# Optimization experiments

Measured on AMD Instinct MI355X. Metric: run time of the kernel, lower is better.

## Reference

```python
import jax, jax.numpy as jnp
import numpy as np

EPS = 0.01  # the module uses 1/sqrt(||x||^2 + 0.01) for cosine normalization


def setup_inputs() -> dict:
    key = jax.random.key(0)
    k1, k2, k3, k4, k5, k6 = jax.random.split(key, 6)
    B, L, L1, D = 512, 256, 256, 128
    sequence = jax.random.randint(k1, (B, L), 0, 10000, dtype=jnp.int32)
    last_sequence = jax.random.randint(k2, (B, L), 0, 2, dtype=jnp.int32)
    sequence_1 = jax.random.randint(k3, (B, L1), 0, 10000, dtype=jnp.int32)
    hist_1 = jax.random.normal(k4, (B, L, D), dtype=jnp.float32)
    hist_2 = jax.random.normal(k5, (B, L1, D), dtype=jnp.float32)
    W = jax.random.normal(k6, (D, D), dtype=jnp.float32) * (1.0 / np.sqrt(D))
    return {"sequence": sequence, "last_sequence": last_sequence,
            "sequence_1": sequence_1, "hist_1": hist_1, "hist_2": hist_2, "W": W}


def reference(sequence, last_sequence, sequence_1, hist_1, hist_2, W):
    # Masks: nonzero ids -> 1.0 (cast to bool then float in the original)
    m = (sequence != 0).astype(jnp.float32)        # [B, L]   key mask for self-attn
    m1 = (sequence_1 != 0).astype(jnp.float32)     # [B, L1]  key mask for cross-attn
    last = last_sequence.astype(jnp.float32)       # [B, L]   last-position indicator

    # --- self cosine-similarity attention over hist_1 ---
    # cos[b,i,j] = <hist_1[b,i], hist_1[b,j]> / (sqrt(||h_i||^2+eps) * sqrt(||h_j||^2+eps))
    dots = jnp.einsum('bid,bjd->bij', hist_1, hist_1)            # [B, L, L]
    inv = jax.lax.rsqrt(jnp.sum(hist_1 * hist_1, axis=-1) + EPS)  # [B, L]
    cos = dots * inv[:, :, None] * inv[:, None, :]
    # softmax-style weighting: exp(cos) masked over keys j (unnormalized exp, per original)
    w = jnp.exp(cos) * m[:, None, :]                             # [B, L, L]
    wsum = jnp.sum(w, axis=-1)                                   # [B, L]
    h_self = jnp.einsum('bij,bjd->bid', w, hist_1) / wsum[..., None]  # [B, L, D]

    # residual add, mask by query validity, then pool at the 'last' position
    h_all_add = (h_self + hist_1) * m[..., None]                 # [B, L, D]
    h_last = jnp.sum(h_all_add * last[..., None], axis=1)        # [B, D]

    # --- cross cosine-similarity attention: h_last attends over hist_2 ---
    dots2 = jnp.einsum('bkd,bd->bk', hist_2, h_last)             # [B, L1]
    inv2k = jax.lax.rsqrt(jnp.sum(hist_2 * hist_2, axis=-1) + EPS)  # [B, L1]
    inv2q = jax.lax.rsqrt(jnp.sum(h_last * h_last, axis=-1) + EPS)  # [B]
    cos2 = dots2 * inv2k * inv2q[:, None]
    w2 = jnp.exp(cos2) * m1                                      # [B, L1]
    h = jnp.einsum('bk,bkd->bd', w2, hist_2) / jnp.sum(w2, axis=-1, keepdims=True)

    out = jax.nn.relu(h @ W)                                     # [B, D]
    return out.reshape(-1, 1, W.shape[0])                        # [B, 1, hidden_num]
```

## Files before the change

### kernel.cpp

```cpp
#include <hip/hip_runtime.h>


using u16 = unsigned short;
using u32 = unsigned int;
typedef __attribute__((ext_vector_type(8))) short bf16x8;
typedef __attribute__((ext_vector_type(4))) float f32x4;
typedef __attribute__((ext_vector_type(4))) u32 u32x4;
typedef __attribute__((ext_vector_type(2))) u32 u32x2;

#define KST 136
#define TST 40
#define WSTR 40
#define KBSZ 4352
#define TBSZ 5120

__device__ __forceinline__ u16 f2bf(float f) {
  union { float f; u32 i; } v; v.f = f;
  u32 r = v.i + 0x7FFFu + ((v.i >> 16) & 1u);
  return (u16)(r >> 16);
}
__device__ __forceinline__ bf16x8 as_bf(u32x4 x) {
  union { u32x4 u; bf16x8 b; } c; c.u = x; return c.b;
}
__device__ __forceinline__ u32x4 pack_bf8(const float* p, float& ss) {
  const float4 a = *(const float4*)p;
  const float4 c = *(const float4*)(p + 4);
  ss += a.x*a.x + a.y*a.y + a.z*a.z + a.w*a.w
      + c.x*c.x + c.y*c.y + c.z*c.z + c.w*c.w;
  u32x4 v;
  v.x = (u32)f2bf(a.x) | ((u32)f2bf(a.y) << 16);
  v.y = (u32)f2bf(a.z) | ((u32)f2bf(a.w) << 16);
  v.z = (u32)f2bf(c.x) | ((u32)f2bf(c.y) << 16);
  v.w = (u32)f2bf(c.z) | ((u32)f2bf(c.w) << 16);
  return v;
}
__device__ __forceinline__ u32x4 packpair(float4 a, float4 c) {
  u32x4 v;
  v.x = (u32)f2bf(a.x) | ((u32)f2bf(a.y) << 16);
  v.y = (u32)f2bf(a.z) | ((u32)f2bf(a.w) << 16);
  v.z = (u32)f2bf(c.x) | ((u32)f2bf(c.y) << 16);
  v.w = (u32)f2bf(c.z) | ((u32)f2bf(c.w) << 16);
  return v;
}

__device__ __forceinline__ void stage_tile(u32x4 v, float ss, u16* kb, u16* tb,
                                           float* invt, int wv, int q, int m16) {
  const int row = wv * 4 + q;
  *(u32x4*)&kb[row * KST + m16 * 8] = v;
  ss += __shfl_xor(ss, 1); ss += __shfl_xor(ss, 2);
  ss += __shfl_xor(ss, 4); ss += __shfl_xor(ss, 8);
  if (m16 == 0) invt[row] = rsqrtf(ss + 0.01f);
  u32 w0 = v.x, w1 = v.y, w2 = v.z, w3 = v.w;
  {
    const int s1 = q & 1;
    u32 xa = s1 ? w0 : w1;
    u32 xb = s1 ? w2 : w3;
    xa = __shfl_xor(xa, 16);
    xb = __shfl_xor(xb, 16);
    if (s1) { w0 = xa; w2 = xb; } else { w1 = xa; w3 = xb; }
    const int s2 = q >> 1;
    u32 ya = s2 ? w0 : w2;
    u32 yb = s2 ? w1 : w3;
    ya = __shfl_xor(ya, 32);
    yb = __shfl_xor(yb, 32);
    if (s2) { w0 = ya; w1 = yb; } else { w2 = ya; w3 = yb; }
  }
  const int d0   = m16 * 8 + q * 2;
  const int base = wv * 4;
  u32x2 lo; lo.x = (w0 & 0xffffu) | (w1 << 16); lo.y = (w2 & 0xffffu) | (w3 << 16);
  u32x2 hi; hi.x = (w0 >> 16) | (w1 & 0xffff0000u); hi.y = (w2 >> 16) | (w3 & 0xffff0000u);
  *(u32x2*)&tb[d0 * TST + base]       = lo;
  *(u32x2*)&tb[(d0 + 1) * TST + base] = hi;
}

__launch_bounds__(512)
__global__ void itd_fused(const int* __restrict__ seq,
                          const int* __restrict__ lastseq,
                          const int* __restrict__ seq1,
                          const float* __restrict__ h1g,
                          const float* __restrict__ h2g,
                          const float* __restrict__ wg,
                          float* __restrict__ outg) {
  __shared__ unsigned long long SBIG[4736];
  __shared__ u16 WST[8][2 * 16 * WSTR];
  __shared__ float MK[256], LM[256], HLacc[128], HH[128], INVT[64], SC[2];

  u16* const  Kb  = (u16*)SBIG;
  u16* const  Tb  = (u16*)SBIG + 2 * KBSZ;
  float* const PSC = (float*)SBIG;

  const int b    = blockIdx.x;
  const int t    = threadIdx.x;
  const int lane = t & 63;
  const int wv   = t >> 6;
  const int q    = lane >> 4;
  const int m16  = lane & 15;

  const float* h1b = h1g + (size_t)b * 32768;

  if (t < 128) HLacc[t] = 0.f;
  if (t < 256) {
    float m = (seq[b * 256 + t] != 0) ? 1.f : 0.f;
    MK[t] = m;
    LM[t] = m * (float)lastseq[b * 256 + t];
  }

  u32x4 av[2][4];
  float invi[2][4];
  #pragma unroll
  for (int rt = 0; rt < 2; ++rt) {
    const int i0 = wv * 32 + rt * 16;
    float ss = 0.f;
    #pragma unroll
    for (int s = 0; s < 4; ++s)
      av[rt][s] = pack_bf8(&h1b[(i0 + m16) * 128 + s * 32 + q * 8], ss);
    ss += __shfl_xor(ss, 16);
    ss += __shfl_xor(ss, 32);
    const float invrow = rsqrtf(ss + 0.01f);
    #pragma unroll
    for (int r = 0; r < 4; ++r) invi[rt][r] = __shfl(invrow, q * 4 + r);
  }

  __syncthreads();

  const int srow = t >> 4;
  const int scol = (t & 15) * 8;
  float4 rpA = {0.f, 0.f, 0.f, 0.f};
  float4 rpB = {0.f, 0.f, 0.f, 0.f};
  {
    const float4 a0 = *(const float4*)&h1b[srow * 128 + scol];
    const float4 c0 = *(const float4*)&h1b[srow * 128 + scol + 4];
    const float lm0 = LM[srow];
    rpA.x += lm0 * a0.x; rpA.y += lm0 * a0.y; rpA.z += lm0 * a0.z; rpA.w += lm0 * a0.w;
    rpB.x += lm0 * c0.x; rpB.y += lm0 * c0.y; rpB.z += lm0 * c0.z; rpB.w += lm0 * c0.w;
    float ss = a0.x*a0.x + a0.y*a0.y + a0.z*a0.z + a0.w*a0.w
             + c0.x*c0.x + c0.y*c0.y + c0.z*c0.z + c0.w*c0.w;
    stage_tile(packpair(a0, c0), ss, Kb, Tb, INVT, wv, q, m16);
  }
  __syncthreads();

  const f32x4 fz = {0.f, 0.f, 0.f, 0.f};
  f32x4 acc[2][8];
  #pragma unroll
  for (int rt = 0; rt < 2; ++rt)
    #pragma unroll
    for (int dt = 0; dt < 8; ++dt) acc[rt][dt] = fz;
  float wpart[2][4] = {{0.f,0.f,0.f,0.f},{0.f,0.f,0.f,0.f}};
  u16* wst0 = &WST[wv][0];
  u16* wst1 = &WST[wv][16 * WSTR];

  for (int jt = 0; jt < 8; ++jt) {
    const int cur = jt & 1;
    float4 pfa, pfb;
    if (jt < 7) {
      const float* np = &h1b[(jt + 1) * 4096 + srow * 128 + scol];
      pfa = *(const float4*)np;
      pfb = *(const float4*)(np + 4);
    }

    f32x4 Sa[2] = {fz, fz}, Sb[2] = {fz, fz};
    const u16* kb = Kb + cur * KBSZ;
    #pragma unroll
    for (int s = 0; s < 4; ++s) {
      bf16x8 ba = *(const bf16x8*)&kb[m16 * KST + s * 32 + q * 8];
      bf16x8 bb = *(const bf16x8*)&kb[(16 + m16) * KST + s * 32 + q * 8];
      bf16x8 a0 = as_bf(av[0][s]);
      bf16x8 a1 = as_bf(av[1][s]);
      Sa[0] = __builtin_amdgcn_mfma_f32_16x16x32_bf16(a0, ba, Sa[0], 0, 0, 0);
      Sb[0] = __builtin_amdgcn_mfma_f32_16x16x32_bf16(a0, bb, Sb[0], 0, 0, 0);
      Sa[1] = __builtin_amdgcn_mfma_f32_16x16x32_bf16(a1, ba, Sa[1], 0, 0, 0);
      Sb[1] = __builtin_amdgcn_mfma_f32_16x16x32_bf16(a1, bb, Sb[1], 0, 0, 0);
    }
    const float invja = INVT[cur * 32 + m16];
    const float invjb = INVT[cur * 32 + 16 + m16];
    const float mja = MK[jt * 32 + m16];
    const float mjb = MK[jt * 32 + 16 + m16];
    #pragma unroll
    for (int rt = 0; rt < 2; ++rt) {
      u16* wr = rt ? wst1 : wst0;
      #pragma unroll
      for (int r = 0; r < 4; ++r) {
        const float wa = __expf(Sa[rt][r] * (invi[rt][r] * invja)) * mja;
        const float wb = __expf(Sb[rt][r] * (invi[rt][r] * invjb)) * mjb;
        wpart[rt][r] += wa + wb;
        wr[(q * 4 + r) * WSTR + m16]      = f2bf(wa);
        wr[(q * 4 + r) * WSTR + 16 + m16] = f2bf(wb);
      }
    }
    __threadfence_block();
    const bf16x8 aw0 = *(const bf16x8*)&wst0[m16 * WSTR + q * 8];
    const bf16x8 aw1 = *(const bf16x8*)&wst1[m16 * WSTR + q * 8];
    const u16* tb = Tb + cur * TBSZ;
    #pragma unroll
    for (int dt = 0; dt < 8; ++dt) {
      const bf16x8 bt = *(const bf16x8*)&tb[(dt * 16 + m16) * TST + q * 8];
      acc[0][dt] = __builtin_amdgcn_mfma_f32_16x16x32_bf16(aw0, bt, acc[0][dt], 0, 0, 0);
      acc[1][dt] = __builtin_amdgcn_mfma_f32_16x16x32_bf16(aw1, bt, acc[1][dt], 0, 0, 0);
    }
    if (jt < 7) {
      const float lmrow = LM[(jt + 1) * 32 + srow];
      rpA.x += lmrow * pfa.x; rpA.y += lmrow * pfa.y;
      rpA.z += lmrow * pfa.z; rpA.w += lmrow * pfa.w;
      rpB.x += lmrow * pfb.x; rpB.y += lmrow * pfb.y;
      rpB.z += lmrow * pfb.z; rpB.w += lmrow * pfb.w;
      float ss = pfa.x*pfa.x + pfa.y*pfa.y + pfa.z*pfa.z + pfa.w*pfa.w
               + pfb.x*pfb.x + pfb.y*pfb.y + pfb.z*pfb.z + pfb.w*pfb.w;
      stage_tile(packpair(pfa, pfb), ss,
                 Kb + (cur ^ 1) * KBSZ, Tb + (cur ^ 1) * TBSZ,
                 INVT + (cur ^ 1) * 32, wv, q, m16);
    }
    __syncthreads();
  }

  #pragma unroll
  for (int rt = 0; rt < 2; ++rt) {
    const int i0 = wv * 32 + rt * 16;
    float rws[4];
    #pragma unroll
    for (int r = 0; r < 4; ++r) {
      float s = wpart[rt][r];
      s += __shfl_xor(s, 1); s += __shfl_xor(s, 2);
      s += __shfl_xor(s, 4); s += __shfl_xor(s, 8);
      rws[r] = 1.f / s;
    }
    #pragma unroll
    for (int dt = 0; dt < 8; ++dt) {
      float v = 0.f;
      #pragma unroll
      for (int r = 0; r < 4; ++r)
        v += acc[rt][dt][r] * rws[r] * LM[i0 + q * 4 + r];
      v += __shfl_xor(v, 16);
      v += __shfl_xor(v, 32);
      if (q == 0) atomicAdd(&HLacc[dt * 16 + m16], v);
    }
  }

  *(float4*)&PSC[srow * 132 + scol]     = rpA;
  *(float4*)&PSC[srow * 132 + scol + 4] = rpB;
  __syncthreads();
  if (t < 128) {
    float s = 0.f;
    #pragma unroll 8
    for (int n = 0; n < 32; ++n) s += PSC[n * 132 + t];
    HLacc[t] += s;
  }
  __syncthreads();

  if (t < 64) {
    float s = HLacc[t] * HLacc[t] + HLacc[t + 64] * HLacc[t + 64];
    s += __shfl_xor(s, 1); s += __shfl_xor(s, 2); s += __shfl_xor(s, 4);
    s += __shfl_xor(s, 8); s += __shfl_xor(s, 16); s += __shfl_xor(s, 32);
    if (t == 0) SC[0] = rsqrtf(s + 0.01f);
  }
  if (t < 256) MK[t] = (seq1[b * 256 + t] != 0) ? 1.f : 0.f;
  __syncthreads();

  const float* h2b = h2g + (size_t)b * 32768;
  {
    const int row8 = lane >> 3;
    const int sub  = lane & 7;
    const int slot = wv * 8 + row8;
    const float invq = SC[0];
    float4 acc4[4];
    #pragma unroll
    for (int c = 0; c < 4; ++c) acc4[c] = {0.f, 0.f, 0.f, 0.f};
    float ws2 = 0.f;
    const float* hl = &HLacc[sub * 4];
    #pragma unroll
    for (int kt = 0; kt < 4; ++kt) {
      const int k = kt * 64 + slot;
      const float* rowp = h2b + k * 128 + sub * 4;
      const float4 v0 = *(const float4*)(rowp);
      const float4 v1 = *(const float4*)(rowp + 32);
      const float4 v2 = *(const float4*)(rowp + 64);
      const float4 v3 = *(const float4*)(rowp + 96);
      float dot = v0.x*hl[0]  + v0.y*hl[1]  + v0.z*hl[2]  + v0.w*hl[3]
                + v1.x*hl[32] + v1.y*hl[33] + v1.z*hl[34] + v1.w*hl[35]
                + v2.x*hl[64] + v2.y*hl[65] + v2.z*hl[66] + v2.w*hl[67]
                + v3.x*hl[96] + v3.y*hl[97] + v3.z*hl[98] + v3.w*hl[99];
      float ss  = v0.x*v0.x + v0.y*v0.y + v0.z*v0.z + v0.w*v0.w
                + v1.x*v1.x + v1.y*v1.y + v1.z*v1.z + v1.w*v1.w
                + v2.x*v2.x + v2.y*v2.y + v2.z*v2.z + v2.w*v2.w
                + v3.x*v3.x + v3.y*v3.y + v3.z*v3.z + v3.w*v3.w;
      dot += __shfl_xor(dot, 1); dot += __shfl_xor(dot, 2); dot += __shfl_xor(dot, 4);
      ss  += __shfl_xor(ss, 1);  ss  += __shfl_xor(ss, 2);  ss  += __shfl_xor(ss, 4);
      const float w2 = __expf(dot * rsqrtf(ss + 0.01f) * invq) * MK[k];
      ws2 += w2;
      acc4[0].x += w2*v0.x; acc4[0].y += w2*v0.y; acc4[0].z += w2*v0.z; acc4[0].w += w2*v0.w;
      acc4[1].x += w2*v1.x; acc4[1].y += w2*v1.y; acc4[1].z += w2*v1.z; acc4[1].w += w2*v1.w;
      acc4[2].x += w2*v2.x; acc4[2].y += w2*v2.y; acc4[2].z += w2*v2.z; acc4[2].w += w2*v2.w;
      acc4[3].x += w2*v3.x; acc4[3].y += w2*v3.y; acc4[3].z += w2*v3.z; acc4[3].w += w2*v3.w;
    }
    #pragma unroll
    for (int c = 0; c < 4; ++c)
      *(float4*)&PSC[slot * 132 + c * 32 + sub * 4] = acc4[c];
    if (sub == 0) INVT[slot] = ws2;
  }
  __syncthreads();

  float hsum = 0.f;
  if (t < 128) {
    #pragma unroll 8
    for (int n = 0; n < 64; ++n) hsum += PSC[n * 132 + t];
  }
  if (t < 64) {
    float s = INVT[t];
    s += __shfl_xor(s, 1); s += __shfl_xor(s, 2); s += __shfl_xor(s, 4);
    s += __shfl_xor(s, 8); s += __shfl_xor(s, 16); s += __shfl_xor(s, 32);
    if (t == 0) SC[1] = s;
  }
  __syncthreads();
  if (t < 128) HH[t] = hsum / SC[1];
  __syncthreads();

  if (t < 128) {
    float o = 0.f;
    #pragma unroll 8
    for (int d = 0; d < 128; ++d)
      o += HH[d] * wg[d * 128 + t];
    outg[(size_t)b * 128 + t] = fmaxf(o, 0.f);
  }
}

extern "C" void kernel_launch(void* const* d_in, const int* in_sizes, int n_in,
                              void* d_out, int out_size, void* d_ws, size_t ws_size,
                              hipStream_t stream) {
  (void)in_sizes; (void)n_in; (void)d_ws; (void)ws_size; (void)out_size;
  const int*   seq     = (const int*)d_in[0];
  const int*   lastseq = (const int*)d_in[1];
  const int*   seq1    = (const int*)d_in[2];
  const float* h1      = (const float*)d_in[3];
  const float* h2      = (const float*)d_in[4];
  const float* w       = (const float*)d_in[5];
  float* out           = (float*)d_out;
  itd_fused<<<dim3(512), dim3(512), 0, stream>>>(seq, lastseq, seq1, h1, h2, w, out);
}
```

Baseline: 204.3 us.

## Split fused kernel into two-block self-attention plus separate cross-attention kernel

The single fused 512-thread kernel per batch becomes two kernels. The first runs two 256-thread blocks per batch, each owning half of the query rows, with a single-buffered key tile and launch bounds that allow four blocks per CU. The second does the cross-attention and output projection after combining the two partial pooled vectors through the workspace. The goal is more parallelism and higher occupancy from smaller blocks and less shared memory. The cost is a second launch, a round-trip through global memory, loss of the double-buffered prefetch overlap, and reading each batch's key tiles twice (once per block).

```diff
diff --git a/kernel.cpp b/kernel.cpp
--- a/kernel.cpp
+++ b/kernel.cpp
@@ -11,8 +11,6 @@
 #define KST 136
 #define TST 40
 #define WSTR 40
-#define KBSZ 4352
-#define TBSZ 5120
 
 __device__ __forceinline__ u16 f2bf(float f) {
   union { float f; u32 i; } v; v.f = f;
@@ -21,18 +19,6 @@
 }
 __device__ __forceinline__ bf16x8 as_bf(u32x4 x) {
   union { u32x4 u; bf16x8 b; } c; c.u = x; return c.b;
-}
-__device__ __forceinline__ u32x4 pack_bf8(const float* p, float& ss) {
-  const float4 a = *(const float4*)p;
-  const float4 c = *(const float4*)(p + 4);
-  ss += a.x*a.x + a.y*a.y + a.z*a.z + a.w*a.w
-      + c.x*c.x + c.y*c.y + c.z*c.z + c.w*c.w;
-  u32x4 v;
-  v.x = (u32)f2bf(a.x) | ((u32)f2bf(a.y) << 16);
-  v.y = (u32)f2bf(a.z) | ((u32)f2bf(a.w) << 16);
-  v.z = (u32)f2bf(c.x) | ((u32)f2bf(c.y) << 16);
-  v.w = (u32)f2bf(c.z) | ((u32)f2bf(c.w) << 16);
-  return v;
 }
 __device__ __forceinline__ u32x4 packpair(float4 a, float4 c) {
   u32x4 v;
@@ -42,10 +28,18 @@
   v.w = (u32)f2bf(c.z) | ((u32)f2bf(c.w) << 16);
   return v;
 }
-
-__device__ __forceinline__ void stage_tile(u32x4 v, float ss, u16* kb, u16* tb,
-                                           float* invt, int wv, int q, int m16) {
-  const int row = wv * 4 + q;
+__device__ __forceinline__ u32x4 pack_bf8(const float* p, float& ss) {
+  const float4 a = *(const float4*)p;
+  const float4 c = *(const float4*)(p + 4);
+  ss += a.x*a.x + a.y*a.y + a.z*a.z + a.w*a.w
+      + c.x*c.x + c.y*c.y + c.z*c.z + c.w*c.w;
+  return packpair(a, c);
+}
+
+__device__ __forceinline__ void stage_half(u32x4 v, float ss, int ro,
+                                           u16* kb, u16* tb, float* invt,
+                                           int wv, int q, int m16) {
+  const int row = ro + wv * 4 + q;
   *(u32x4*)&kb[row * KST + m16 * 8] = v;
   ss += __shfl_xor(ss, 1); ss += __shfl_xor(ss, 2);
   ss += __shfl_xor(ss, 4); ss += __shfl_xor(ss, 8);
@@ -66,30 +60,29 @@
     if (s2) { w0 = ya; w1 = yb; } else { w2 = ya; w3 = yb; }
   }
   const int d0   = m16 * 8 + q * 2;
-  const int base = wv * 4;
+  const int base = ro + wv * 4;
   u32x2 lo; lo.x = (w0 & 0xffffu) | (w1 << 16); lo.y = (w2 & 0xffffu) | (w3 << 16);
   u32x2 hi; hi.x = (w0 >> 16) | (w1 & 0xffff0000u); hi.y = (w2 >> 16) | (w3 & 0xffff0000u);
   *(u32x2*)&tb[d0 * TST + base]       = lo;
   *(u32x2*)&tb[(d0 + 1) * TST + base] = hi;
 }
 
-__launch_bounds__(512)
-__global__ void itd_fused(const int* __restrict__ seq,
-                          const int* __restrict__ lastseq,
-                          const int* __restrict__ seq1,
-                          const float* __restrict__ h1g,
-                          const float* __restrict__ h2g,
-                          const float* __restrict__ wg,
-                          float* __restrict__ outg) {
-  __shared__ unsigned long long SBIG[4736];
-  __shared__ u16 WST[8][2 * 16 * WSTR];
-  __shared__ float MK[256], LM[256], HLacc[128], HH[128], INVT[64], SC[2];
-
-  u16* const  Kb  = (u16*)SBIG;
-  u16* const  Tb  = (u16*)SBIG + 2 * KBSZ;
-  float* const PSC = (float*)SBIG;
-
-  const int b    = blockIdx.x;
+__launch_bounds__(256, 4)
+__global__ void itd_self(const int* __restrict__ seq,
+                         const int* __restrict__ lastseq,
+                         const float* __restrict__ h1g,
+                         float* __restrict__ hlws) {
+  __shared__ u16 SB[9472];
+  __shared__ u16 WST[4][2 * 16 * WSTR];
+  __shared__ float MK[256], LM[256], HLacc[128], INVT[32];
+
+  u16* const Kb = SB;
+  u16* const Tb = SB + 32 * KST;
+  float* const PSC = (float*)SB;
+
+  const int bid  = blockIdx.x;
+  const int p    = bid & 1;
+  const int b    = bid >> 1;
   const int t    = threadIdx.x;
   const int lane = t & 63;
   const int wv   = t >> 6;
@@ -99,7 +92,7 @@
   const float* h1b = h1g + (size_t)b * 32768;
 
   if (t < 128) HLacc[t] = 0.f;
-  if (t < 256) {
+  {
     float m = (seq[b * 256 + t] != 0) ? 1.f : 0.f;
     MK[t] = m;
     LM[t] = m * (float)lastseq[b * 256 + t];
@@ -109,7 +102,7 @@
   float invi[2][4];
   #pragma unroll
   for (int rt = 0; rt < 2; ++rt) {
-    const int i0 = wv * 32 + rt * 16;
+    const int i0 = p * 128 + wv * 32 + rt * 16;
     float ss = 0.f;
     #pragma unroll
     for (int s = 0; s < 4; ++s)
@@ -120,24 +113,15 @@
     #pragma unroll
     for (int r = 0; r < 4; ++r) invi[rt][r] = __shfl(invrow, q * 4 + r);
   }
-
   __syncthreads();
 
   const int srow = t >> 4;
   const int scol = (t & 15) * 8;
-  float4 rpA = {0.f, 0.f, 0.f, 0.f};
-  float4 rpB = {0.f, 0.f, 0.f, 0.f};
-  {
-    const float4 a0 = *(const float4*)&h1b[srow * 128 + scol];
-    const float4 c0 = *(const float4*)&h1b[srow * 128 + scol + 4];
-    const float lm0 = LM[srow];
-    rpA.x += lm0 * a0.x; rpA.y += lm0 * a0.y; rpA.z += lm0 * a0.z; rpA.w += lm0 * a0.w;
-    rpB.x += lm0 * c0.x; rpB.y += lm0 * c0.y; rpB.z += lm0 * c0.z; rpB.w += lm0 * c0.w;
-    float ss = a0.x*a0.x + a0.y*a0.y + a0.z*a0.z + a0.w*a0.w
-             + c0.x*c0.x + c0.y*c0.y + c0.z*c0.z + c0.w*c0.w;
-    stage_tile(packpair(a0, c0), ss, Kb, Tb, INVT, wv, q, m16);
-  }
-  __syncthreads();
+
+  float4 a0 = *(const float4*)&h1b[srow * 128 + scol];
+  float4 c0 = *(const float4*)&h1b[srow * 128 + scol + 4];
+  float4 a1 = *(const float4*)&h1b[(16 + srow) * 128 + scol];
+  float4 c1 = *(const float4*)&h1b[(16 + srow) * 128 + scol + 4];
 
   const f32x4 fz = {0.f, 0.f, 0.f, 0.f};
   f32x4 acc[2][8];
@@ -146,33 +130,51 @@
     #pragma unroll
     for (int dt = 0; dt < 8; ++dt) acc[rt][dt] = fz;
   float wpart[2][4] = {{0.f,0.f,0.f,0.f},{0.f,0.f,0.f,0.f}};
+  f32x4 rpA = fz, rpB = fz;
   u16* wst0 = &WST[wv][0];
   u16* wst1 = &WST[wv][16 * WSTR];
 
   for (int jt = 0; jt < 8; ++jt) {
-    const int cur = jt & 1;
-    float4 pfa, pfb;
+    if ((jt & 1) == p) {
+      const float lm0 = LM[jt * 32 + srow];
+      const float lm1 = LM[jt * 32 + 16 + srow];
+      rpA[0] += lm0*a0.x + lm1*a1.x; rpA[1] += lm0*a0.y + lm1*a1.y;
+      rpA[2] += lm0*a0.z + lm1*a1.z; rpA[3] += lm0*a0.w + lm1*a1.w;
+      rpB[0] += lm0*c0.x + lm1*c1.x; rpB[1] += lm0*c0.y + lm1*c1.y;
+      rpB[2] += lm0*c0.z + lm1*c1.z; rpB[3] += lm0*c0.w + lm1*c1.w;
+    }
+    {
+      float ss0 = a0.x*a0.x + a0.y*a0.y + a0.z*a0.z + a0.w*a0.w
+                + c0.x*c0.x + c0.y*c0.y + c0.z*c0.z + c0.w*c0.w;
+      stage_half(packpair(a0, c0), ss0, 0, Kb, Tb, INVT, wv, q, m16);
+      float ss1 = a1.x*a1.x + a1.y*a1.y + a1.z*a1.z + a1.w*a1.w
+                + c1.x*c1.x + c1.y*c1.y + c1.z*c1.z + c1.w*c1.w;
+      stage_half(packpair(a1, c1), ss1, 16, Kb, Tb, INVT, wv, q, m16);
+    }
+    __syncthreads();
+
     if (jt < 7) {
       const float* np = &h1b[(jt + 1) * 4096 + srow * 128 + scol];
-      pfa = *(const float4*)np;
-      pfb = *(const float4*)(np + 4);
+      a0 = *(const float4*)np;
+      c0 = *(const float4*)(np + 4);
+      a1 = *(const float4*)(np + 2048);
+      c1 = *(const float4*)(np + 2052);
     }
 
     f32x4 Sa[2] = {fz, fz}, Sb[2] = {fz, fz};
-    const u16* kb = Kb + cur * KBSZ;
     #pragma unroll
     for (int s = 0; s < 4; ++s) {
-      bf16x8 ba = *(const bf16x8*)&kb[m16 * KST + s * 32 + q * 8];
-      bf16x8 bb = *(const bf16x8*)&kb[(16 + m16) * KST + s * 32 + q * 8];
-      bf16x8 a0 = as_bf(av[0][s]);
-      bf16x8 a1 = as_bf(av[1][s]);
-      Sa[0] = __builtin_amdgcn_mfma_f32_16x16x32_bf16(a0, ba, Sa[0], 0, 0, 0);
-      Sb[0] = __builtin_amdgcn_mfma_f32_16x16x32_bf16(a0, bb, Sb[0], 0, 0, 0);
-      Sa[1] = __builtin_amdgcn_mfma_f32_16x16x32_bf16(a1, ba, Sa[1], 0, 0, 0);
-      Sb[1] = __builtin_amdgcn_mfma_f32_16x16x32_bf16(a1, bb, Sb[1], 0, 0, 0);
-    }
-    const float invja = INVT[cur * 32 + m16];
-    const float invjb = INVT[cur * 32 + 16 + m16];
+      bf16x8 ba = *(const bf16x8*)&Kb[m16 * KST + s * 32 + q * 8];
+      bf16x8 bb = *(const bf16x8*)&Kb[(16 + m16) * KST + s * 32 + q * 8];
+      bf16x8 af0 = as_bf(av[0][s]);
+      bf16x8 af1 = as_bf(av[1][s]);
+      Sa[0] = __builtin_amdgcn_mfma_f32_16x16x32_bf16(af0, ba, Sa[0], 0, 0, 0);
+      Sb[0] = __builtin_amdgcn_mfma_f32_16x16x32_bf16(af0, bb, Sb[0], 0, 0, 0);
+      Sa[1] = __builtin_amdgcn_mfma_f32_16x16x32_bf16(af1, ba, Sa[1], 0, 0, 0);
+      Sb[1] = __builtin_amdgcn_mfma_f32_16x16x32_bf16(af1, bb, Sb[1], 0, 0, 0);
+    }
+    const float invja = INVT[m16];
+    const float invjb = INVT[16 + m16];
     const float mja = MK[jt * 32 + m16];
     const float mjb = MK[jt * 32 + 16 + m16];
     #pragma unroll
@@ -190,31 +192,18 @@
     __threadfence_block();
     const bf16x8 aw0 = *(const bf16x8*)&wst0[m16 * WSTR + q * 8];
     const bf16x8 aw1 = *(const bf16x8*)&wst1[m16 * WSTR + q * 8];
-    const u16* tb = Tb + cur * TBSZ;
     #pragma unroll
     for (int dt = 0; dt < 8; ++dt) {
-      const bf16x8 bt = *(const bf16x8*)&tb[(dt * 16 + m16) * TST + q * 8];
+      const bf16x8 bt = *(const bf16x8*)&Tb[(dt * 16 + m16) * TST + q * 8];
       acc[0][dt] = __builtin_amdgcn_mfma_f32_16x16x32_bf16(aw0, bt, acc[0][dt], 0, 0, 0);
       acc[1][dt] = __builtin_amdgcn_mfma_f32_16x16x32_bf16(aw1, bt, acc[1][dt], 0, 0, 0);
     }
-    if (jt < 7) {
-      const float lmrow = LM[(jt + 1) * 32 + srow];
-      rpA.x += lmrow * pfa.x; rpA.y += lmrow * pfa.y;
-      rpA.z += lmrow * pfa.z; rpA.w += lmrow * pfa.w;
-      rpB.x += lmrow * pfb.x; rpB.y += lmrow * pfb.y;
-      rpB.z += lmrow * pfb.z; rpB.w += lmrow * pfb.w;
-      float ss = pfa.x*pfa.x + pfa.y*pfa.y + pfa.z*pfa.z + pfa.w*pfa.w
-               + pfb.x*pfb.x + pfb.y*pfb.y + pfb.z*pfb.z + pfb.w*pfb.w;
-      stage_tile(packpair(pfa, pfb), ss,
-                 Kb + (cur ^ 1) * KBSZ, Tb + (cur ^ 1) * TBSZ,
-                 INVT + (cur ^ 1) * 32, wv, q, m16);
-    }
     __syncthreads();
   }
 
   #pragma unroll
   for (int rt = 0; rt < 2; ++rt) {
-    const int i0 = wv * 32 + rt * 16;
+    const int i0 = p * 128 + wv * 32 + rt * 16;
     float rws[4];
     #pragma unroll
     for (int r = 0; r < 4; ++r) {
@@ -235,24 +224,40 @@
     }
   }
 
-  *(float4*)&PSC[srow * 132 + scol]     = rpA;
-  *(float4*)&PSC[srow * 132 + scol + 4] = rpB;
+  *(f32x4*)&PSC[srow * 132 + scol]     = rpA;
+  *(f32x4*)&PSC[srow * 132 + scol + 4] = rpB;
   __syncthreads();
   if (t < 128) {
     float s = 0.f;
-    #pragma unroll 8
-    for (int n = 0; n < 32; ++n) s += PSC[n * 132 + t];
-    HLacc[t] += s;
-  }
+    #pragma unroll
+    for (int n = 0; n < 16; ++n) s += PSC[n * 132 + t];
+    hlws[(size_t)b * 256 + p * 128 + t] = HLacc[t] + s;
+  }
+}
+
+__launch_bounds__(256)
+__global__ void itd_cross(const int* __restrict__ seq1,
+                          const float* __restrict__ h2g,
+                          const float* __restrict__ wg,
+                          const float* __restrict__ hlws,
+                          float* __restrict__ outg) {
+  __shared__ float HL[128], MK1[256], PSC[32 * 132], WS2[32], SC[2], HH[128];
+
+  const int b    = blockIdx.x;
+  const int t    = threadIdx.x;
+  const int lane = t & 63;
+  const int wv   = t >> 6;
+
+  if (t < 128) HL[t] = hlws[(size_t)b * 256 + t] + hlws[(size_t)b * 256 + 128 + t];
+  MK1[t] = (seq1[b * 256 + t] != 0) ? 1.f : 0.f;
   __syncthreads();
 
   if (t < 64) {
-    float s = HLacc[t] * HLacc[t] + HLacc[t + 64] * HLacc[t + 64];
+    float s = HL[t] * HL[t] + HL[t + 64] * HL[t + 64];
     s += __shfl_xor(s, 1); s += __shfl_xor(s, 2); s += __shfl_xor(s, 4);
     s += __shfl_xor(s, 8); s += __shfl_xor(s, 16); s += __shfl_xor(s, 32);
     if (t == 0) SC[0] = rsqrtf(s + 0.01f);
   }
-  if (t < 256) MK[t] = (seq1[b * 256 + t] != 0) ? 1.f : 0.f;
   __syncthreads();
 
   const float* h2b = h2g + (size_t)b * 32768;
@@ -261,14 +266,14 @@
     const int sub  = lane & 7;
     const int slot = wv * 8 + row8;
     const float invq = SC[0];
-    float4 acc4[4];
+    f32x4 acc4[4];
     #pragma unroll
     for (int c = 0; c < 4; ++c) acc4[c] = {0.f, 0.f, 0.f, 0.f};
     float ws2 = 0.f;
-    const float* hl = &HLacc[sub * 4];
-    #pragma unroll
-    for (int kt = 0; kt < 4; ++kt) {
-      const int k = kt * 64 + slot;
+    const float* hl = &HL[sub * 4];
+    #pragma unroll
+    for (int kt = 0; kt < 8; ++kt) {
+      const int k = kt * 32 + slot;
       const float* rowp = h2b + k * 128 + sub * 4;
       const float4 v0 = *(const float4*)(rowp);
       const float4 v1 = *(const float4*)(rowp + 32);
@@ -284,29 +289,29 @@
                 + v3.x*v3.x + v3.y*v3.y + v3.z*v3.z + v3.w*v3.w;
       dot += __shfl_xor(dot, 1); dot += __shfl_xor(dot, 2); dot += __shfl_xor(dot, 4);
       ss  += __shfl_xor(ss, 1);  ss  += __shfl_xor(ss, 2);  ss  += __shfl_xor(ss, 4);
-      const float w2 = __expf(dot * rsqrtf(ss + 0.01f) * invq) * MK[k];
+      const float w2 = __expf(dot * rsqrtf(ss + 0.01f) * invq) * MK1[k];
       ws2 += w2;
-      acc4[0].x += w2*v0.x; acc4[0].y += w2*v0.y; acc4[0].z += w2*v0.z; acc4[0].w += w2*v0.w;
-      acc4[1].x += w2*v1.x; acc4[1].y += w2*v1.y; acc4[1].z += w2*v1.z; acc4[1].w += w2*v1.w;
-      acc4[2].x += w2*v2.x; acc4[2].y += w2*v2.y; acc4[2].z += w2*v2.z; acc4[2].w += w2*v2.w;
-      acc4[3].x += w2*v3.x; acc4[3].y += w2*v3.y; acc4[3].z += w2*v3.z; acc4[3].w += w2*v3.w;
+      acc4[0][0] += w2*v0.x; acc4[0][1] += w2*v0.y; acc4[0][2] += w2*v0.z; acc4[0][3] += w2*v0.w;
+      acc4[1][0] += w2*v1.x; acc4[1][1] += w2*v1.y; acc4[1][2] += w2*v1.z; acc4[1][3] += w2*v1.w;
+      acc4[2][0] += w2*v2.x; acc4[2][1] += w2*v2.y; acc4[2][2] += w2*v2.z; acc4[2][3] += w2*v2.w;
+      acc4[3][0] += w2*v3.x; acc4[3][1] += w2*v3.y; acc4[3][2] += w2*v3.z; acc4[3][3] += w2*v3.w;
     }
     #pragma unroll
     for (int c = 0; c < 4; ++c)
-      *(float4*)&PSC[slot * 132 + c * 32 + sub * 4] = acc4[c];
-    if (sub == 0) INVT[slot] = ws2;
+      *(f32x4*)&PSC[slot * 132 + c * 32 + sub * 4] = acc4[c];
+    if (sub == 0) WS2[slot] = ws2;
   }
   __syncthreads();
 
   float hsum = 0.f;
   if (t < 128) {
-    #pragma unroll 8
-    for (int n = 0; n < 64; ++n) hsum += PSC[n * 132 + t];
-  }
-  if (t < 64) {
-    float s = INVT[t];
+    #pragma unroll
+    for (int n = 0; n < 32; ++n) hsum += PSC[n * 132 + t];
+  }
+  if (t < 32) {
+    float s = WS2[t];
     s += __shfl_xor(s, 1); s += __shfl_xor(s, 2); s += __shfl_xor(s, 4);
-    s += __shfl_xor(s, 8); s += __shfl_xor(s, 16); s += __shfl_xor(s, 32);
+    s += __shfl_xor(s, 8); s += __shfl_xor(s, 16);
     if (t == 0) SC[1] = s;
   }
   __syncthreads();
@@ -325,7 +330,7 @@
 extern "C" void kernel_launch(void* const* d_in, const int* in_sizes, int n_in,
                               void* d_out, int out_size, void* d_ws, size_t ws_size,
                               hipStream_t stream) {
-  (void)in_sizes; (void)n_in; (void)d_ws; (void)ws_size; (void)out_size;
+  (void)in_sizes; (void)n_in; (void)ws_size; (void)out_size;
   const int*   seq     = (const int*)d_in[0];
   const int*   lastseq = (const int*)d_in[1];
   const int*   seq1    = (const int*)d_in[2];
@@ -333,5 +338,7 @@
   const float* h2      = (const float*)d_in[4];
   const float* w       = (const float*)d_in[5];
   float* out           = (float*)d_out;
-  itd_fused<<<dim3(512), dim3(512), 0, stream>>>(seq, lastseq, seq1, h1, h2, w, out);
-}
+  float* hlws          = (float*)d_ws;
+  itd_self<<<dim3(1024), dim3(256), 0, stream>>>(seq, lastseq, h1, hlws);
+  itd_cross<<<dim3(512), dim3(256), 0, stream>>>(seq1, h2, w, hlws, out);
+}
```

Result: slower. 301.5 us (+47.6%).

## Double block size to 1024 threads, one 16-row query tile per wave

Applied to the files above, without the earlier changes.

The fused kernel now launches 1024 threads per block, and each of the 16 waves owns a single 16-row query tile instead of two. This halves the per-wave MFMA work, score registers and accumulators in the self-attention loop. Tile staging, the last-position pooling and the cross-attention stage still run on the first 512 threads only. The intent is more waves per CU for latency hiding and lower register pressure. The cost is more threads sitting idle in the staging and cross-attention phases, and heavier barrier and shared-memory traffic.

```diff
diff --git a/kernel.cpp b/kernel.cpp
--- a/kernel.cpp
+++ b/kernel.cpp
@@ -21,18 +21,6 @@
 }
 __device__ __forceinline__ bf16x8 as_bf(u32x4 x) {
   union { u32x4 u; bf16x8 b; } c; c.u = x; return c.b;
-}
-__device__ __forceinline__ u32x4 pack_bf8(const float* p, float& ss) {
-  const float4 a = *(const float4*)p;
-  const float4 c = *(const float4*)(p + 4);
-  ss += a.x*a.x + a.y*a.y + a.z*a.z + a.w*a.w
-      + c.x*c.x + c.y*c.y + c.z*c.z + c.w*c.w;
-  u32x4 v;
-  v.x = (u32)f2bf(a.x) | ((u32)f2bf(a.y) << 16);
-  v.y = (u32)f2bf(a.z) | ((u32)f2bf(a.w) << 16);
-  v.z = (u32)f2bf(c.x) | ((u32)f2bf(c.y) << 16);
-  v.w = (u32)f2bf(c.z) | ((u32)f2bf(c.w) << 16);
-  return v;
 }
 __device__ __forceinline__ u32x4 packpair(float4 a, float4 c) {
   u32x4 v;
@@ -41,6 +29,13 @@
   v.z = (u32)f2bf(c.x) | ((u32)f2bf(c.y) << 16);
   v.w = (u32)f2bf(c.z) | ((u32)f2bf(c.w) << 16);
   return v;
+}
+__device__ __forceinline__ u32x4 pack_bf8(const float* p, float& ss) {
+  const float4 a = *(const float4*)p;
+  const float4 c = *(const float4*)(p + 4);
+  ss += a.x*a.x + a.y*a.y + a.z*a.z + a.w*a.w
+      + c.x*c.x + c.y*c.y + c.z*c.z + c.w*c.w;
+  return packpair(a, c);
 }
 
 __device__ __forceinline__ void stage_tile(u32x4 v, float ss, u16* kb, u16* tb,
@@ -73,7 +68,7 @@
   *(u32x2*)&tb[(d0 + 1) * TST + base] = hi;
 }
 
-__launch_bounds__(512)
+__launch_bounds__(1024, 4)
 __global__ void itd_fused(const int* __restrict__ seq,
                           const int* __restrict__ lastseq,
                           const int* __restrict__ seq1,
@@ -82,11 +77,12 @@
                           const float* __restrict__ wg,
                           float* __restrict__ outg) {
   __shared__ unsigned long long SBIG[4736];
-  __shared__ u16 WST[8][2 * 16 * WSTR];
-  __shared__ float MK[256], LM[256], HLacc[128], HH[128], INVT[64], SC[2];
-
-  u16* const  Kb  = (u16*)SBIG;
-  u16* const  Tb  = (u16*)SBIG + 2 * KBSZ;
+  __shared__ u16 WST[16][16 * WSTR];
+  __shared__ float MK[256], LM[256], HLacc[128], HH[128];
+  __shared__ float INVT[2][32], WS2[64], SC[2];
+
+  u16* const Kb  = (u16*)SBIG;
+  u16* const Tb  = (u16*)SBIG + 2 * KBSZ;
   float* const PSC = (float*)SBIG;
 
   const int b    = blockIdx.x;
@@ -105,120 +101,102 @@
     LM[t] = m * (float)lastseq[b * 256 + t];
   }
 
-  u32x4 av[2][4];
-  float invi[2][4];
-  #pragma unroll
-  for (int rt = 0; rt < 2; ++rt) {
-    const int i0 = wv * 32 + rt * 16;
+  const int i0 = wv * 16;
+  u32x4 av[4];
+  float invi[4];
+  {
     float ss = 0.f;
     #pragma unroll
     for (int s = 0; s < 4; ++s)
-      av[rt][s] = pack_bf8(&h1b[(i0 + m16) * 128 + s * 32 + q * 8], ss);
+      av[s] = pack_bf8(&h1b[(i0 + m16) * 128 + s * 32 + q * 8], ss);
     ss += __shfl_xor(ss, 16);
     ss += __shfl_xor(ss, 32);
     const float invrow = rsqrtf(ss + 0.01f);
     #pragma unroll
-    for (int r = 0; r < 4; ++r) invi[rt][r] = __shfl(invrow, q * 4 + r);
-  }
-
-  __syncthreads();
-
-  const int srow = t >> 4;
-  const int scol = (t & 15) * 8;
-  float4 rpA = {0.f, 0.f, 0.f, 0.f};
-  float4 rpB = {0.f, 0.f, 0.f, 0.f};
-  {
+    for (int r = 0; r < 4; ++r) invi[r] = __shfl(invrow, q * 4 + r);
+  }
+  __syncthreads();
+
+  const int srow = wv * 4 + q;
+  const int scol = m16 * 8;
+  const f32x4 fz = {0.f, 0.f, 0.f, 0.f};
+  f32x4 rpA = fz, rpB = fz;
+  if (t < 512) {
     const float4 a0 = *(const float4*)&h1b[srow * 128 + scol];
     const float4 c0 = *(const float4*)&h1b[srow * 128 + scol + 4];
     const float lm0 = LM[srow];
-    rpA.x += lm0 * a0.x; rpA.y += lm0 * a0.y; rpA.z += lm0 * a0.z; rpA.w += lm0 * a0.w;
-    rpB.x += lm0 * c0.x; rpB.y += lm0 * c0.y; rpB.z += lm0 * c0.z; rpB.w += lm0 * c0.w;
+    rpA[0] += lm0 * a0.x; rpA[1] += lm0 * a0.y; rpA[2] += lm0 * a0.z; rpA[3] += lm0 * a0.w;
+    rpB[0] += lm0 * c0.x; rpB[1] += lm0 * c0.y; rpB[2] += lm0 * c0.z; rpB[3] += lm0 * c0.w;
     float ss = a0.x*a0.x + a0.y*a0.y + a0.z*a0.z + a0.w*a0.w
              + c0.x*c0.x + c0.y*c0.y + c0.z*c0.z + c0.w*c0.w;
-    stage_tile(packpair(a0, c0), ss, Kb, Tb, INVT, wv, q, m16);
-  }
-  __syncthreads();
-
-  const f32x4 fz = {0.f, 0.f, 0.f, 0.f};
-  f32x4 acc[2][8];
+    stage_tile(packpair(a0, c0), ss, Kb, Tb, INVT[0], wv, q, m16);
+  }
+  __syncthreads();
+
+  f32x4 acc[8];
   #pragma unroll
-  for (int rt = 0; rt < 2; ++rt)
-    #pragma unroll
-    for (int dt = 0; dt < 8; ++dt) acc[rt][dt] = fz;
-  float wpart[2][4] = {{0.f,0.f,0.f,0.f},{0.f,0.f,0.f,0.f}};
-  u16* wst0 = &WST[wv][0];
-  u16* wst1 = &WST[wv][16 * WSTR];
+  for (int dt = 0; dt < 8; ++dt) acc[dt] = fz;
+  float wpart[4] = {0.f, 0.f, 0.f, 0.f};
+  u16* wst = &WST[wv][0];
 
   for (int jt = 0; jt < 8; ++jt) {
     const int cur = jt & 1;
     float4 pfa, pfb;
-    if (jt < 7) {
+    if (t < 512 && jt < 7) {
       const float* np = &h1b[(jt + 1) * 4096 + srow * 128 + scol];
       pfa = *(const float4*)np;
       pfb = *(const float4*)(np + 4);
     }
 
-    f32x4 Sa[2] = {fz, fz}, Sb[2] = {fz, fz};
+    f32x4 Sa = fz, Sb = fz;
     const u16* kb = Kb + cur * KBSZ;
     #pragma unroll
     for (int s = 0; s < 4; ++s) {
       bf16x8 ba = *(const bf16x8*)&kb[m16 * KST + s * 32 + q * 8];
       bf16x8 bb = *(const bf16x8*)&kb[(16 + m16) * KST + s * 32 + q * 8];
-      bf16x8 a0 = as_bf(av[0][s]);
-      bf16x8 a1 = as_bf(av[1][s]);
-      Sa[0] = __builtin_amdgcn_mfma_f32_16x16x32_bf16(a0, ba, Sa[0], 0, 0, 0);
-      Sb[0] = __builtin_amdgcn_mfma_f32_16x16x32_bf16(a0, bb, Sb[0], 0, 0, 0);
-      Sa[1] = __builtin_amdgcn_mfma_f32_16x16x32_bf16(a1, ba, Sa[1], 0, 0, 0);
-      Sb[1] = __builtin_amdgcn_mfma_f32_16x16x32_bf16(a1, bb, Sb[1], 0, 0, 0);
-    }
-    const float invja = INVT[cur * 32 + m16];
-    const float invjb = INVT[cur * 32 + 16 + m16];
+      bf16x8 af = as_bf(av[s]);
+      Sa = __builtin_amdgcn_mfma_f32_16x16x32_bf16(af, ba, Sa, 0, 0, 0);
+      Sb = __builtin_amdgcn_mfma_f32_16x16x32_bf16(af, bb, Sb, 0, 0, 0);
+    }
+    const float invja = INVT[cur][m16];
+    const float invjb = INVT[cur][16 + m16];
     const float mja = MK[jt * 32 + m16];
     const float mjb = MK[jt * 32 + 16 + m16];
     #pragma unroll
-    for (int rt = 0; rt < 2; ++rt) {
-      u16* wr = rt ? wst1 : wst0;
-      #pragma unroll
-      for (int r = 0; r < 4; ++r) {
-        const float wa = __expf(Sa[rt][r] * (invi[rt][r] * invja)) * mja;
-        const float wb = __expf(Sb[rt][r] * (invi[rt][r] * invjb)) * mjb;
-        wpart[rt][r] += wa + wb;
-        wr[(q * 4 + r) * WSTR + m16]      = f2bf(wa);
-        wr[(q * 4 + r) * WSTR + 16 + m16] = f2bf(wb);
-      }
+    for (int r = 0; r < 4; ++r) {
+      const float wa = __expf(Sa[r] * (invi[r] * invja)) * mja;
+      const float wb = __expf(Sb[r] * (invi[r] * invjb)) * mjb;
+      wpart[r] += wa + wb;
+      wst[(q * 4 + r) * WSTR + m16]      = f2bf(wa);
+      wst[(q * 4 + r) * WSTR + 16 + m16] = f2bf(wb);
     }
     __threadfence_block();
-    const bf16x8 aw0 = *(const bf16x8*)&wst0[m16 * WSTR + q * 8];
-    const bf16x8 aw1 = *(const bf16x8*)&wst1[m16 * WSTR + q * 8];
+    const bf16x8 aw = *(const bf16x8*)&wst[m16 * WSTR + q * 8];
     const u16* tb = Tb + cur * TBSZ;
     #pragma unroll
     for (int dt = 0; dt < 8; ++dt) {
       const bf16x8 bt = *(const bf16x8*)&tb[(dt * 16 + m16) * TST + q * 8];
-      acc[0][dt] = __builtin_amdgcn_mfma_f32_16x16x32_bf16(aw0, bt, acc[0][dt], 0, 0, 0);
-      acc[1][dt] = __builtin_amdgcn_mfma_f32_16x16x32_bf16(aw1, bt, acc[1][dt], 0, 0, 0);
-    }
-    if (jt < 7) {
+      acc[dt] = __builtin_amdgcn_mfma_f32_16x16x32_bf16(aw, bt, acc[dt], 0, 0, 0);
+    }
+    if (t < 512 && jt < 7) {
       const float lmrow = LM[(jt + 1) * 32 + srow];
-      rpA.x += lmrow * pfa.x; rpA.y += lmrow * pfa.y;
-      rpA.z += lmrow * pfa.z; rpA.w += lmrow * pfa.w;
-      rpB.x += lmrow * pfb.x; rpB.y += lmrow * pfb.y;
-      rpB.z += lmrow * pfb.z; rpB.w += lmrow * pfb.w;
+      rpA[0] += lmrow * pfa.x; rpA[1] += lmrow * pfa.y;
+      rpA[2] += lmrow * pfa.z; rpA[3] += lmrow * pfa.w;
+      rpB[0] += lmrow * pfb.x; rpB[1] += lmrow * pfb.y;
+      rpB[2] += lmrow * pfb.z; rpB[3] += lmrow * pfb.w;
       float ss = pfa.x*pfa.x + pfa.y*pfa.y + pfa.z*pfa.z + pfa.w*pfa.w
                + pfb.x*pfb.x + pfb.y*pfb.y + pfb.z*pfb.z + pfb.w*pfb.w;
-      stage_tile(packpair(pfa, pfb), ss,
-                 Kb + (cur ^ 1) * KBSZ, Tb + (cur ^ 1) * TBSZ,
-                 INVT + (cur ^ 1) * 32, wv, q, m16);
+      stage_tile(packpair(pfa, pfb), ss, Kb + (cur ^ 1) * KBSZ,
+                 Tb + (cur ^ 1) * TBSZ, INVT[cur ^ 1], wv, q, m16);
     }
     __syncthreads();
   }
 
-  #pragma unroll
-  for (int rt = 0; rt < 2; ++rt) {
-    const int i0 = wv * 32 + rt * 16;
+  {
     float rws[4];
     #pragma unroll
     for (int r = 0; r < 4; ++r) {
-      float s = wpart[rt][r];
+      float s = wpart[r];
       s += __shfl_xor(s, 1); s += __shfl_xor(s, 2);
       s += __shfl_xor(s, 4); s += __shfl_xor(s, 8);
       rws[r] = 1.f / s;
@@ -228,19 +206,21 @@
       float v = 0.f;
       #pragma unroll
       for (int r = 0; r < 4; ++r)
-        v += acc[rt][dt][r] * rws[r] * LM[i0 + q * 4 + r];
+        v += acc[dt][r] * rws[r] * LM[i0 + q * 4 + r];
       v += __shfl_xor(v, 16);
       v += __shfl_xor(v, 32);
       if (q == 0) atomicAdd(&HLacc[dt * 16 + m16], v);
     }
   }
 
-  *(float4*)&PSC[srow * 132 + scol]     = rpA;
-  *(float4*)&PSC[srow * 132 + scol + 4] = rpB;
+  if (t < 512) {
+    *(f32x4*)&PSC[srow * 132 + scol]     = rpA;
+    *(f32x4*)&PSC[srow * 132 + scol + 4] = rpB;
+  }
   __syncthreads();
   if (t < 128) {
     float s = 0.f;
-    #pragma unroll 8
+    #pragma unroll
     for (int n = 0; n < 32; ++n) s += PSC[n * 132 + t];
     HLacc[t] += s;
   }
@@ -256,14 +236,14 @@
   __syncthreads();
 
   const float* h2b = h2g + (size_t)b * 32768;
-  {
+  if (t < 512) {
     const int row8 = lane >> 3;
     const int sub  = lane & 7;
     const int slot = wv * 8 + row8;
     const float invq = SC[0];
-    float4 acc4[4];
-    #pragma unroll
-    for (int c = 0; c < 4; ++c) acc4[c] = {0.f, 0.f, 0.f, 0.f};
+    f32x4 acc4[4];
+    #pragma unroll
+    for (int c = 0; c < 4; ++c) acc4[c] = fz;
     float ws2 = 0.f;
     const float* hl = &HLacc[sub * 4];
     #pragma unroll
@@ -286,25 +266,25 @@
       ss  += __shfl_xor(ss, 1);  ss  += __shfl_xor(ss, 2);  ss  += __shfl_xor(ss, 4);
       const float w2 = __expf(dot * rsqrtf(ss + 0.01f) * invq) * MK[k];
       ws2 += w2;
-      acc4[0].x += w2*v0.x; acc4[0].y += w2*v0.y; acc4[0].z += w2*v0.z; acc4[0].w += w2*v0.w;
-      acc4[1].x += w2*v1.x; acc4[1].y += w2*v1.y; acc4[1].z += w2*v1.z; acc4[1].w += w2*v1.w;
-      acc4[2].x += w2*v2.x; acc4[2].y += w2*v2.y; acc4[2].z += w2*v2.z; acc4[2].w += w2*v2.w;
-      acc4[3].x += w2*v3.x; acc4[3].y += w2*v3.y; acc4[3].z += w2*v3.z; acc4[3].w += w2*v3.w;
+      acc4[0][0] += w2*v0.x; acc4[0][1] += w2*v0.y; acc4[0][2] += w2*v0.z; acc4[0][3] += w2*v0.w;
+      acc4[1][0] += w2*v1.x; acc4[1][1] += w2*v1.y; acc4[1][2] += w2*v1.z; acc4[1][3] += w2*v1.w;
+      acc4[2][0] += w2*v2.x; acc4[2][1] += w2*v2.y; acc4[2][2] += w2*v2.z; acc4[2][3] += w2*v2.w;
+      acc4[3][0] += w2*v3.x; acc4[3][1] += w2*v3.y; acc4[3][2] += w2*v3.z; acc4[3][3] += w2*v3.w;
     }
     #pragma unroll
     for (int c = 0; c < 4; ++c)
-      *(float4*)&PSC[slot * 132 + c * 32 + sub * 4] = acc4[c];
-    if (sub == 0) INVT[slot] = ws2;
+      *(f32x4*)&PSC[slot * 132 + c * 32 + sub * 4] = acc4[c];
+    if (sub == 0) WS2[slot] = ws2;
   }
   __syncthreads();
 
   float hsum = 0.f;
   if (t < 128) {
-    #pragma unroll 8
+    #pragma unroll
     for (int n = 0; n < 64; ++n) hsum += PSC[n * 132 + t];
   }
   if (t < 64) {
-    float s = INVT[t];
+    float s = WS2[t];
     s += __shfl_xor(s, 1); s += __shfl_xor(s, 2); s += __shfl_xor(s, 4);
     s += __shfl_xor(s, 8); s += __shfl_xor(s, 16); s += __shfl_xor(s, 32);
     if (t == 0) SC[1] = s;
@@ -333,5 +313,5 @@
   const float* h2      = (const float*)d_in[4];
   const float* w       = (const float*)d_in[5];
   float* out           = (float*)d_out;
-  itd_fused<<<dim3(512), dim3(512), 0, stream>>>(seq, lastseq, seq1, h1, h2, w, out);
-}
+  itd_fused<<<dim3(512), dim3(1024), 0, stream>>>(seq, lastseq, seq1, h1, h2, w, out);
+}
```

New measurement: 205.0 us. No clear change (+0.4%).
